# Optimization experiments

Hardware: AMD Instinct MI355X
Metric: run time of the kernel (lower is better)

Reference implementation:

```python
import jax, jax.numpy as jnp
import numpy as np

N0, N1, N2 = 100000, 25000, 6250
E0, E1, E2 = 600000, 150000, 37500
K = 6


def cheb_conv(x, edge_index, W, b):
    """torch_geometric ChebConv with sym normalization, lambda_max=2:
    L_hat = -D^{-1/2} A D^{-1/2}; T0=x, T1=L_hat x, Tk=2 L_hat T_{k-1} - T_{k-2}."""
    n = x.shape[0]
    src, dst = edge_index[0], edge_index[1]
    deg = jax.ops.segment_sum(jnp.ones(src.shape[0], x.dtype), src, num_segments=n)
    dinv = jnp.where(deg > 0, jax.lax.rsqrt(jnp.maximum(deg, 1.0)), 0.0)
    w = -(dinv[src] * dinv[dst])  # [E]

    def prop(h):  # (L_hat h)_i = sum_{j->i} w_ij h_j
        return jax.ops.segment_sum(w[:, None] * h[src], dst, num_segments=n)

    Tx0 = x
    out = Tx0 @ W[0]
    Tx1 = prop(x)
    out = out + Tx1 @ W[1]
    for k in range(2, W.shape[0]):
        Tx2 = 2.0 * prop(Tx1) - Tx0
        out = out + Tx2 @ W[k]
        Tx0, Tx1 = Tx1, Tx2
    return out + b


def pool(x, rows, cols, vals, n_out):
    # sparse.mm(D, x): y[r] += v * x[c]
    return jax.ops.segment_sum(vals[:, None] * x[cols], rows, num_segments=n_out)


def setup_inputs() -> dict:
    key = jax.random.key(0)
    ks = jax.random.split(key, 16)
    inp = {}
    inp["x"] = jax.random.normal(ks[0], (N0, 3), jnp.float32)
    inp["edge_index0"] = jax.random.randint(ks[1], (2, E0), 0, N0, jnp.int32)
    inp["edge_index1"] = jax.random.randint(ks[2], (2, E1), 0, N1, jnp.int32)
    inp["edge_index2"] = jax.random.randint(ks[3], (2, E2), 0, N2, jnp.int32)
    s = 0.05
    inp["W0"] = jax.random.normal(ks[4], (K, 3, 128), jnp.float32) * s
    inp["b0"] = jax.random.normal(ks[5], (128,), jnp.float32) * s
    inp["W1"] = jax.random.normal(ks[6], (K, 128, 128), jnp.float32) * s
    inp["b1"] = jax.random.normal(ks[7], (128,), jnp.float32) * s
    inp["W2"] = jax.random.normal(ks[8], (K, 128, 256), jnp.float32) * s
    inp["b2"] = jax.random.normal(ks[9], (256,), jnp.float32) * s
    inp["D0_rows"] = jax.random.randint(ks[10], (100000,), 0, N1, jnp.int32)
    inp["D0_cols"] = jax.random.randint(ks[11], (100000,), 0, N0, jnp.int32)
    inp["D0_vals"] = jax.random.uniform(ks[12], (100000,), jnp.float32)
    inp["D1_rows"] = jax.random.randint(ks[13], (25000,), 0, N2, jnp.int32)
    inp["D1_cols"] = jax.random.randint(ks[14], (25000,), 0, N1, jnp.int32)
    inp["D1_vals"] = jax.random.uniform(ks[15], (25000,), jnp.float32)
    k2 = jax.random.split(jax.random.fold_in(key, 1), 2)
    inp["linW"] = jax.random.normal(k2[0], (10, N2 * 256), jnp.float32) * 0.001
    inp["linb"] = jax.random.normal(k2[1], (10,), jnp.float32) * s
    return inp


def reference(x, edge_index0, edge_index1, edge_index2, W0, b0, W1, b1, W2, b2,
              D0_rows, D0_cols, D0_vals, D1_rows, D1_cols, D1_vals, linW, linb):
    h = jax.nn.relu(cheb_conv(x, edge_index0, W0, b0))      # [N0,128]
    h = pool(h, D0_rows, D0_cols, D0_vals, N1)               # [N1,128]
    h = jax.nn.relu(cheb_conv(h, edge_index1, W1, b1))      # [N1,128]
    h = pool(h, D1_rows, D1_cols, D1_vals, N2)               # [N2,128]
    h = cheb_conv(h, edge_index2, W2, b2)                    # [N2,256]
    Z = linW @ h.reshape(-1) + linb                           # [10]
    return Z
```

## Files before the change

### kernel.cpp

```cpp
#include <hip/hip_runtime.h>


namespace {
constexpr int cN0 = 100000, cN1 = 25000, cN2 = 6250;
constexpr int cE0 = 600000, cE1 = 150000, cE2 = 37500;
constexpr int cD  = cN2 * 256;

constexpr int JN[8]  = {cN0, cN1, cN2, cN1, cN2, cN0, cN1, cN2};
constexpr int JE[8]  = {cE0, cE1, cE2, 100000, 25000, cE0, cE1, cE2};
constexpr int JB[8]  = {391, 98, 25, 98, 25, 391, 98, 25};
constexpr int JBBASE[9] = {0, 391, 489, 514, 612, 637, 1028, 1126, 1151};
constexpr int TB = 1151;
constexpr int JCB[8] = {293, 74, 19, 49, 13, 293, 74, 19};
constexpr int JCBASE[9] = {0, 293, 367, 386, 435, 448, 741, 815, 834};
constexpr int TCB = 834;
constexpr int CHUNK = 2048;
constexpr int BSTRIDE = 400;

constexpr int EBASE[5]   = {0, 600000, 750000, 787500, 887500};
constexpr int E_TOTAL    = 912500;
constexpr int SBASE[3]   = {0, 600000, 750000};
constexpr int S_TOTAL    = 787500;
constexpr int NBASE[5]   = {0, 100096, 125184, 131584, 156672};
constexpr int NPAD_TOTAL = 163072;
constexpr int DEGBASE[3] = {0, 100000, 125000};
constexpr int DEG_TOTAL  = 131250;
}

typedef __attribute__((ext_vector_type(8))) short short8;
typedef __attribute__((ext_vector_type(4))) float floatx4;

__device__ inline ushort f2bf(float f) {
  union { float f; unsigned u; } v; v.f = f;
  unsigned u = v.u;
  return (ushort)((u + 0x7FFFu + ((u >> 16) & 1u)) >> 16);
}

__device__ inline int job_of_cb(int cb) {
  int j = 0;
  while (cb >= JCBASE[j + 1]) ++j;
  return j;
}
__device__ inline int job_of_bucket(int g) {
  int j = 0;
  while (g >= JBBASE[j + 1]) ++j;
  return j;
}

__global__ __launch_bounds__(256) void c1_count_kernel(
    const int* __restrict__ k0, const int* __restrict__ k1, const int* __restrict__ k2,
    const int* __restrict__ k3, const int* __restrict__ k4, const int* __restrict__ k5,
    const int* __restrict__ k6, const int* __restrict__ k7,
    int* __restrict__ cntCB) {
  __shared__ int cnt[BSTRIDE];
  int cb = blockIdx.x;
  int j = job_of_cb(cb);
  int lb = cb - JCBASE[j];
  const int* keys;
  switch (j) {
    case 0: keys = k0; break; case 1: keys = k1; break; case 2: keys = k2; break;
    case 3: keys = k3; break; case 4: keys = k4; break; case 5: keys = k5; break;
    case 6: keys = k6; break; default: keys = k7; break;
  }
  int nB = JB[j];
  for (int b = threadIdx.x; b < nB; b += 256) cnt[b] = 0;
  __syncthreads();
  int e0 = lb * CHUNK;
  int e1 = min(e0 + CHUNK, JE[j]);
  for (int e = e0 + threadIdx.x; e < e1; e += 256)
    atomicAdd(&cnt[keys[e] >> 8], 1);
  __syncthreads();
  for (int b = threadIdx.x; b < nB; b += 256)
    cntCB[cb * BSTRIDE + b] = cnt[b];
}

__global__ __launch_bounds__(256) void c2a_scan_kernel(int* __restrict__ cntCB,
                                                       int* __restrict__ bucketTot) {
  __shared__ int s[256];
  int g = blockIdx.x;
  int j = job_of_bucket(g);
  int b = g - JBBASE[j];
  int cb0 = JCBASE[j], nCB = JCB[j];
  int carry = 0;
  for (int c0 = 0; c0 < nCB; c0 += 256) {
    int i = c0 + threadIdx.x;
    int v = (i < nCB) ? cntCB[(cb0 + i) * BSTRIDE + b] : 0;
    s[threadIdx.x] = v;
    __syncthreads();
    for (int d = 1; d < 256; d <<= 1) {
      int t = (threadIdx.x >= d) ? s[threadIdx.x - d] : 0;
      __syncthreads();
      s[threadIdx.x] += t;
      __syncthreads();
    }
    if (i < nCB) cntCB[(cb0 + i) * BSTRIDE + b] = carry + s[threadIdx.x] - v;
    carry += s[255];
    __syncthreads();
  }
  if (threadIdx.x == 0) bucketTot[g] = carry;
}

__global__ __launch_bounds__(256) void c2b_scan_kernel(const int* __restrict__ bucketTot,
                                                       int* __restrict__ bucketBase) {
  __shared__ int s[256];
  int j = blockIdx.x;
  int g0 = JBBASE[j], nB = JB[j];
  int carry = 0;
  for (int c0 = 0; c0 < nB; c0 += 256) {
    int i = c0 + threadIdx.x;
    int v = (i < nB) ? bucketTot[g0 + i] : 0;
    s[threadIdx.x] = v;
    __syncthreads();
    for (int d = 1; d < 256; d <<= 1) {
      int t = (threadIdx.x >= d) ? s[threadIdx.x - d] : 0;
      __syncthreads();
      s[threadIdx.x] += t;
      __syncthreads();
    }
    if (i < nB) bucketBase[g0 + i] = carry + s[threadIdx.x] - v;
    carry += s[255];
    __syncthreads();
  }
}

__global__ __launch_bounds__(256) void c3_src_kernel(
    const int* __restrict__ s0, const int* __restrict__ s1, const int* __restrict__ s2,
    const int* __restrict__ cntCB, const int* __restrict__ bucketBase,
    int* __restrict__ scatSrc) {
  __shared__ int base[BSTRIDE];
  int cb = blockIdx.x + JCBASE[5];
  int j = job_of_cb(cb);
  int lb = cb - JCBASE[j];
  const int* keys = (j == 5) ? s0 : (j == 6) ? s1 : s2;
  int nB = JB[j];
  for (int b = threadIdx.x; b < nB; b += 256)
    base[b] = SBASE[j - 5] + bucketBase[JBBASE[j] + b] + cntCB[cb * BSTRIDE + b];
  __syncthreads();
  int e0 = lb * CHUNK;
  int e1 = min(e0 + CHUNK, JE[j]);
  for (int e = e0 + threadIdx.x; e < e1; e += 256) {
    int s = keys[e];
    int pos = atomicAdd(&base[s >> 8], 1);
    scatSrc[pos] = s & 255;
  }
}

__global__ __launch_bounds__(256) void ddeg_kernel(const int* __restrict__ scatSrc,
                                                   const int* __restrict__ bucketTot,
                                                   const int* __restrict__ bucketBase,
                                                   float* __restrict__ dinv) {
  __shared__ int cnt[256];
  int g = blockIdx.x + JBBASE[5];
  int j = job_of_bucket(g);
  int b = g - JBBASE[j];
  int st = SBASE[j - 5] + bucketBase[g];
  int en = st + bucketTot[g];
  cnt[threadIdx.x] = 0;
  __syncthreads();
  for (int idx = st + threadIdx.x; idx < en; idx += 256)
    atomicAdd(&cnt[scatSrc[idx]], 1);
  __syncthreads();
  int node = b * 256 + threadIdx.x;
  if (node < JN[j]) {
    int c = cnt[threadIdx.x];
    dinv[DEGBASE[j - 5] + node] = (c > 0) ? rsqrtf((float)c) : 0.f;
  }
}

__global__ __launch_bounds__(256) void c3_dst_kernel(
    const int* __restrict__ d0, const int* __restrict__ s0,
    const int* __restrict__ d1, const int* __restrict__ s1,
    const int* __restrict__ d2, const int* __restrict__ s2,
    const int* __restrict__ p0r, const int* __restrict__ p0c, const float* __restrict__ p0v,
    const int* __restrict__ p1r, const int* __restrict__ p1c, const float* __restrict__ p1v,
    const float* __restrict__ dinv,
    const int* __restrict__ cntCB, const int* __restrict__ bucketBase,
    int2* __restrict__ scatPairs) {
  __shared__ int base[BSTRIDE];
  int cb = blockIdx.x;
  int j = job_of_cb(cb);
  int lb = cb - JCBASE[j];
  const int* dk; const int* sk; const float* vv = nullptr;
  switch (j) {
    case 0: dk = d0; sk = s0; break;
    case 1: dk = d1; sk = s1; break;
    case 2: dk = d2; sk = s2; break;
    case 3: dk = p0r; sk = p0c; vv = p0v; break;
    default: dk = p1r; sk = p1c; vv = p1v; break;
  }
  int nB = JB[j];
  for (int b = threadIdx.x; b < nB; b += 256)
    base[b] = EBASE[j] + bucketBase[JBBASE[j] + b] + cntCB[cb * BSTRIDE + b];
  __syncthreads();
  int e0 = lb * CHUNK;
  int e1 = min(e0 + CHUNK, JE[j]);
  for (int e = e0 + threadIdx.x; e < e1; e += 256) {
    int d = dk[e];
    int s = sk[e];
    float w;
    if (j < 3) w = -(dinv[DEGBASE[j] + s] * dinv[DEGBASE[j] + d]);
    else w = vv[e];
    int pos = atomicAdd(&base[d >> 8], 1);
    scatPairs[pos] = make_int2(((d & 255) << 17) | s, __float_as_int(w));
  }
}

__global__ __launch_bounds__(256) void dcsr_kernel(const int2* __restrict__ scatPairs,
                                                   const int* __restrict__ bucketTot,
                                                   const int* __restrict__ bucketBase,
                                                   int* __restrict__ off,
                                                   int2* __restrict__ csrPairs) {
  __shared__ int cnt[256];
  __shared__ int sArr[256];
  __shared__ int cur[256];
  int g = blockIdx.x;
  int j = job_of_bucket(g);
  int b = g - JBBASE[j];
  int relBase = bucketBase[g];
  int st = EBASE[j] + relBase;
  int en = st + bucketTot[g];
  cnt[threadIdx.x] = 0;
  __syncthreads();
  for (int idx = st + threadIdx.x; idx < en; idx += 256)
    atomicAdd(&cnt[scatPairs[idx].x >> 17], 1);
  __syncthreads();
  int v = cnt[threadIdx.x];
  sArr[threadIdx.x] = v;
  __syncthreads();
  for (int d = 1; d < 256; d <<= 1) {
    int t = (threadIdx.x >= d) ? sArr[threadIdx.x - d] : 0;
    __syncthreads();
    sArr[threadIdx.x] += t;
    __syncthreads();
  }
  int excl = sArr[threadIdx.x] - v;
  int node = b * 256 + threadIdx.x;
  if (node < JN[j]) off[NBASE[j] + node] = relBase + excl;
  if (threadIdx.x == 0 && b == JB[j] - 1) off[NBASE[j] + JN[j]] = JE[j];
  cur[threadIdx.x] = st + excl;
  __syncthreads();
  for (int idx = st + threadIdx.x; idx < en; idx += 256) {
    int2 p = scatPairs[idx];
    int dl = p.x >> 17;
    int s = p.x & 0x1FFFF;
    int pos = atomicAdd(&cur[dl], 1);
    csrPairs[pos] = make_int2(s, p.y);
  }
}

__global__ __launch_bounds__(256) void csr_prop128_kernel(
    const int* __restrict__ off, const int2* __restrict__ pairs,
    const float* __restrict__ h, float* __restrict__ y, ushort* __restrict__ ybf,
    const float* __restrict__ prev, float scale, int N) {
  int r = blockIdx.x * 8 + (threadIdx.x >> 5);
  int l = threadIdx.x & 31;
  if (r >= N) return;
  int s = off[r], e = off[r + 1];
  const float4* h4 = (const float4*)h;
  float ax = 0.f, ay = 0.f, az = 0.f, aw = 0.f;
  int j = s;
  for (; j + 4 <= e; j += 4) {
    int2 p0 = pairs[j], p1 = pairs[j + 1], p2 = pairs[j + 2], p3 = pairs[j + 3];
    float4 v0 = h4[(size_t)p0.x * 32 + l];
    float4 v1 = h4[(size_t)p1.x * 32 + l];
    float4 v2 = h4[(size_t)p2.x * 32 + l];
    float4 v3 = h4[(size_t)p3.x * 32 + l];
    float w0 = __int_as_float(p0.y), w1 = __int_as_float(p1.y);
    float w2 = __int_as_float(p2.y), w3 = __int_as_float(p3.y);
    ax += w0 * v0.x + w1 * v1.x + w2 * v2.x + w3 * v3.x;
    ay += w0 * v0.y + w1 * v1.y + w2 * v2.y + w3 * v3.y;
    az += w0 * v0.z + w1 * v1.z + w2 * v2.z + w3 * v3.z;
    aw += w0 * v0.w + w1 * v1.w + w2 * v2.w + w3 * v3.w;
  }
  for (; j < e; ++j) {
    int2 p = pairs[j];
    float4 v0 = h4[(size_t)p.x * 32 + l];
    float w = __int_as_float(p.y);
    ax += w * v0.x; ay += w * v0.y; az += w * v0.z; aw += w * v0.w;
  }
  float4 v = make_float4(scale * ax, scale * ay, scale * az, scale * aw);
  if (prev) {
    float4 pv = ((const float4*)prev)[(size_t)r * 32 + l];
    v.x -= pv.x; v.y -= pv.y; v.z -= pv.z; v.w -= pv.w;
  }
  if (y) ((float4*)y)[(size_t)r * 32 + l] = v;
  uint2 sp = make_uint2(f2bf(v.x) | ((unsigned)f2bf(v.y) << 16),
                        f2bf(v.z) | ((unsigned)f2bf(v.w) << 16));
  ((uint2*)ybf)[(size_t)r * 32 + l] = sp;
}

__global__ void csr_prop3_kernel(const int* __restrict__ off, const int2* __restrict__ pairs,
                                 const float4* __restrict__ h, float4* __restrict__ y,
                                 const float4* __restrict__ prev, float scale, int N,
                                 ushort* __restrict__ ybf, int kout) {
  int r = blockIdx.x * blockDim.x + threadIdx.x;
  if (r >= N) return;
  int s = off[r], e = off[r + 1];
  float ax = 0.f, ay = 0.f, az = 0.f;
  int j = s;
  for (; j + 4 <= e; j += 4) {
    int2 p0 = pairs[j], p1 = pairs[j + 1], p2 = pairs[j + 2], p3 = pairs[j + 3];
    float4 h0 = h[p0.x], h1 = h[p1.x], h2 = h[p2.x], h3 = h[p3.x];
    float w0 = __int_as_float(p0.y), w1 = __int_as_float(p1.y);
    float w2 = __int_as_float(p2.y), w3 = __int_as_float(p3.y);
    ax += w0 * h0.x + w1 * h1.x + w2 * h2.x + w3 * h3.x;
    ay += w0 * h0.y + w1 * h1.y + w2 * h2.y + w3 * h3.y;
    az += w0 * h0.z + w1 * h1.z + w2 * h2.z + w3 * h3.z;
  }
  for (; j < e; ++j) {
    int2 p = pairs[j];
    float4 hv = h[p.x];
    float w = __int_as_float(p.y);
    ax += w * hv.x; ay += w * hv.y; az += w * hv.z;
  }
  float4 v = make_float4(scale * ax, scale * ay, scale * az, 0.f);
  if (prev) {
    float4 pv = prev[r];
    v.x -= pv.x; v.y -= pv.y; v.z -= pv.z;
  }
  y[r] = v;
  uint2 sp = make_uint2(f2bf(v.x) | ((unsigned)f2bf(v.y) << 16), (unsigned)f2bf(v.z));
  *(uint2*)(ybf + (size_t)r * 32 + kout * 4) = sp;
}

__global__ void copyx_kernel(const float* __restrict__ x, float4* __restrict__ Tb,
                             ushort* __restrict__ Abf, int N) {
  int r = blockIdx.x * 256 + threadIdx.x;
  if (r >= N) return;
  float x0 = x[3 * r], x1 = x[3 * r + 1], x2 = x[3 * r + 2];
  Tb[r] = make_float4(x0, x1, x2, 0.f);
  uint4 z = make_uint4(0, 0, 0, 0);
  uint4 first = make_uint4(f2bf(x0) | ((unsigned)f2bf(x1) << 16), (unsigned)f2bf(x2), 0, 0);
  uint4* p = (uint4*)(Abf + (size_t)r * 32);
  p[0] = first; p[1] = z; p[2] = z; p[3] = z;
}

__global__ __launch_bounds__(256, 2) void h0_mfma_kernel(
    const ushort* __restrict__ Abf, const ushort* __restrict__ W0b,
    const float* __restrict__ b0, float* __restrict__ h0, int M) {
  __shared__ ushort Al[64][40];
  __shared__ ushort Bl[128][40];
  const int tid = threadIdx.x;
  const int rowBase = blockIdx.x * 64;
  const int wave = tid >> 6;
  const int lane = tid & 63;
  const int m16 = lane & 15;
  const int quad = lane >> 4;
  {
    int sRow = tid >> 2;
    int sK8 = (tid & 3) * 8;
    int row = rowBase + sRow;
    uint4 av = make_uint4(0, 0, 0, 0);
    if (row < M) av = *(const uint4*)(Abf + (size_t)row * 32 + sK8);
    *(uint4*)&Al[sRow][sK8] = av;
  }
#pragma unroll
  for (int l = 0; l < 2; ++l) {
    int lin = tid + l * 256;
    int bRow = lin >> 2;
    int bK8 = (lin & 3) * 8;
    *(uint4*)&Bl[bRow][bK8] = *(const uint4*)(W0b + (size_t)bRow * 32 + bK8);
  }
  __syncthreads();
  short8 a = *(const short8*)&Al[wave * 16 + m16][quad * 8];
  floatx4 acc[8];
#pragma unroll
  for (int c = 0; c < 8; ++c) {
    floatx4 z;
    z[0] = 0.f; z[1] = 0.f; z[2] = 0.f; z[3] = 0.f;
    short8 b = *(const short8*)&Bl[c * 16 + m16][quad * 8];
    acc[c] = __builtin_amdgcn_mfma_f32_16x16x32_bf16(a, b, z, 0, 0, 0);
  }
#pragma unroll
  for (int c = 0; c < 8; ++c) {
    int col = c * 16 + m16;
    float bv = b0[col];
#pragma unroll
    for (int r = 0; r < 4; ++r) {
      int row = rowBase + wave * 16 + quad * 4 + r;
      if (row < M) h0[(size_t)row * 128 + col] = fmaxf(acc[c][r] + bv, 0.f);
    }
  }
}

__global__ void prep_w_kernel(const float* __restrict__ W0, const float* __restrict__ W1,
                              const float* __restrict__ W2, ushort* __restrict__ W0b,
                              ushort* __restrict__ Wt1, ushort* __restrict__ Wt2) {
  int i = blockIdx.x * 256 + threadIdx.x;
  if (i < 768 * 128) {
    int k = i / 128, n = i - k * 128;
    Wt1[(size_t)n * 768 + k] = f2bf(W1[i]);
  } else if (i < 768 * 128 + 768 * 256) {
    int i2 = i - 768 * 128;
    int k = i2 / 256, n = i2 - k * 256;
    Wt2[(size_t)n * 768 + k] = f2bf(W2[i2]);
  } else {
    int i3 = i - 768 * 128 - 768 * 256;
    if (i3 < 128 * 32) {
      int col = i3 >> 5, k = i3 & 31;
      int a = k >> 2, jj = k & 3;
      float v = (k < 24 && jj < 3) ? W0[(a * 3 + jj) * 128 + col] : 0.f;
      W0b[(size_t)col * 32 + k] = f2bf(v);
    }
  }
}

template <int RELU>
__global__ __launch_bounds__(256, 2) void gemm_mfma_kernel(
    const ushort* __restrict__ Tbf, const ushort* __restrict__ Wt,
    const float* __restrict__ bias, float* __restrict__ C, int M, int N) {
  __shared__ ushort Al[64][40];
  __shared__ ushort Bl[128][40];
  const int tid = threadIdx.x;
  const int rowBase = blockIdx.x * 64;
  const int colBase = blockIdx.y * 128;
  const int wave = tid >> 6;
  const int lane = tid & 63;
  const int m16 = lane & 15;
  const int quad = lane >> 4;
  const size_t Mstride = (size_t)M * 128;

  floatx4 acc[8];
#pragma unroll
  for (int c = 0; c < 8; ++c)
#pragma unroll
    for (int r = 0; r < 4; ++r) acc[c][r] = 0.f;

  const int sRow = tid >> 2;
  const int sK8 = (tid & 3) * 8;
  const int growA = rowBase + sRow;
  const bool aValid = growA < M;

  for (int kc = 0; kc < 24; ++kc) {
    uint4 av = make_uint4(0, 0, 0, 0);
    if (aValid)
      av = *(const uint4*)(Tbf + (size_t)(kc >> 2) * Mstride + (size_t)growA * 128
                           + ((kc & 3) << 5) + sK8);
    *(uint4*)&Al[sRow][sK8] = av;
#pragma unroll
    for (int l = 0; l < 2; ++l) {
      int lin = tid + l * 256;
      int bRow = lin >> 2;
      int bK8 = (lin & 3) * 8;
      *(uint4*)&Bl[bRow][bK8] =
          *(const uint4*)(Wt + (size_t)(colBase + bRow) * 768 + kc * 32 + bK8);
    }
    __syncthreads();

    short8 a = *(const short8*)&Al[wave * 16 + m16][quad * 8];
#pragma unroll
    for (int c = 0; c < 8; ++c) {
      short8 b = *(const short8*)&Bl[c * 16 + m16][quad * 8];
      acc[c] = __builtin_amdgcn_mfma_f32_16x16x32_bf16(a, b, acc[c], 0, 0, 0);
    }
    __syncthreads();
  }

#pragma unroll
  for (int c = 0; c < 8; ++c) {
    int col = colBase + c * 16 + m16;
    float bv = bias[col];
#pragma unroll
    for (int r = 0; r < 4; ++r) {
      int row = rowBase + wave * 16 + quad * 4 + r;
      if (row < M) {
        float v = acc[c][r] + bv;
        if (RELU) v = fmaxf(v, 0.f);
        C[(size_t)row * N + col] = v;
      }
    }
  }
}

__global__ void initout_kernel(float* __restrict__ out, const float* __restrict__ linb) {
  int i = threadIdx.x;
  if (i < 10) out[i] = linb[i];
}

__global__ __launch_bounds__(256) void linear_kernel(const float* __restrict__ Wl,
                                                     const float* __restrict__ h,
                                                     float* __restrict__ out, int D) {
  float p[10];
#pragma unroll
  for (int j = 0; j < 10; ++j) p[j] = 0.f;
  int stride = gridDim.x * blockDim.x;
  for (int i = blockIdx.x * blockDim.x + threadIdx.x; i < D; i += stride) {
    float hv = h[i];
#pragma unroll
    for (int j = 0; j < 10; ++j) p[j] += Wl[(size_t)j * D + i] * hv;
  }
#pragma unroll
  for (int j = 0; j < 10; ++j) {
#pragma unroll
    for (int off = 32; off > 0; off >>= 1) p[j] += __shfl_down(p[j], off, 64);
  }
  __shared__ float s[4][10];
  int wave = threadIdx.x >> 6, lane = threadIdx.x & 63;
  if (lane == 0) {
#pragma unroll
    for (int j = 0; j < 10; ++j) s[wave][j] = p[j];
  }
  __syncthreads();
  if (threadIdx.x < 10) {
    float t = s[0][threadIdx.x] + s[1][threadIdx.x] + s[2][threadIdx.x] + s[3][threadIdx.x];
    atomicAdd(&out[threadIdx.x], t);
  }
}

extern "C" void kernel_launch(void* const* d_in, const int* in_sizes, int n_in,
                              void* d_out, int out_size, void* d_ws, size_t ws_size,
                              hipStream_t stream) {
  const float* x    = (const float*)d_in[0];
  const int*   ei0  = (const int*)d_in[1];
  const int*   ei1  = (const int*)d_in[2];
  const int*   ei2  = (const int*)d_in[3];
  const float* W0   = (const float*)d_in[4];
  const float* b0   = (const float*)d_in[5];
  const float* W1   = (const float*)d_in[6];
  const float* b1   = (const float*)d_in[7];
  const float* W2   = (const float*)d_in[8];
  const float* b2   = (const float*)d_in[9];
  const int*   D0r  = (const int*)d_in[10];
  const int*   D0c  = (const int*)d_in[11];
  const float* D0v  = (const float*)d_in[12];
  const int*   D1r  = (const int*)d_in[13];
  const int*   D1c  = (const int*)d_in[14];
  const float* D1v  = (const float*)d_in[15];
  const float* linW = (const float*)d_in[16];
  const float* linb = (const float*)d_in[17];
  float* out = (float*)d_out;
  (void)in_sizes; (void)n_in; (void)out_size; (void)ws_size;

  const int* src0 = ei0;            const int* dst0 = ei0 + cE0;
  const int* src1 = ei1;            const int* dst1 = ei1 + cE1;
  const int* src2 = ei2;            const int* dst2 = ei2 + cE2;

  float* ws = (float*)d_ws;
  size_t off = 0;
  auto alloc = [&](size_t n) {
    float* p = ws + off;
    off += (n + 63) & ~size_t(63);
    return p;
  };
  float* dinv       = alloc(DEG_TOTAL);
  int*   cntCB      = (int*)alloc((size_t)TCB * BSTRIDE);
  int*   bucketTot  = (int*)alloc(TB);
  int*   bucketBase = (int*)alloc(TB);
  int*   scatSrc    = (int*)alloc(S_TOTAL);
  int2*  scatPairs  = (int2*)alloc((size_t)2 * E_TOTAL);
  int2*  csrPairs   = (int2*)alloc((size_t)2 * E_TOTAL);
  int*   offArr     = (int*)alloc(NPAD_TOTAL);
  ushort* W0b       = (ushort*)alloc(128 * 32 / 2);
  ushort* Wt1       = (ushort*)alloc(768 * 128 / 2);
  ushort* Wt2       = (ushort*)alloc(768 * 256 / 2);
  float4* Tb0       = (float4*)alloc((size_t)6 * cN0 * 4);
  ushort* Abf0      = (ushort*)alloc((size_t)cN0 * 16);
  float* h0buf      = alloc((size_t)cN0 * 128);
  float* Tlvl1      = alloc((size_t)6 * cN1 * 128);
  ushort* Tbf1      = (ushort*)alloc((size_t)6 * cN1 * 64);
  float* out1       = alloc((size_t)cN1 * 128);
  float* Tlvl2      = alloc((size_t)6 * cN2 * 128);
  ushort* Tbf2      = (ushort*)alloc((size_t)6 * cN2 * 64);
  float* out2       = alloc((size_t)cN2 * 256);

  auto nb = [](long long n) { return (unsigned)((n + 255) / 256); };

  c1_count_kernel<<<TCB, 256, 0, stream>>>(dst0, dst1, dst2, D0r, D1r,
                                           src0, src1, src2, cntCB);
  c2a_scan_kernel<<<TB, 256, 0, stream>>>(cntCB, bucketTot);
  c2b_scan_kernel<<<8, 256, 0, stream>>>(bucketTot, bucketBase);
  c3_src_kernel<<<TCB - JCBASE[5], 256, 0, stream>>>(src0, src1, src2,
                                                     cntCB, bucketBase, scatSrc);
  ddeg_kernel<<<TB - JBBASE[5], 256, 0, stream>>>(scatSrc, bucketTot, bucketBase, dinv);
  c3_dst_kernel<<<JCBASE[5], 256, 0, stream>>>(dst0, src0, dst1, src1, dst2, src2,
                                               D0r, D0c, D0v, D1r, D1c, D1v,
                                               dinv, cntCB, bucketBase, scatPairs);
  dcsr_kernel<<<JBBASE[5], 256, 0, stream>>>(scatPairs, bucketTot, bucketBase,
                                             offArr, csrPairs);
  prep_w_kernel<<<nb(768 * 384 + 128 * 32), 256, 0, stream>>>(W0, W1, W2, W0b, Wt1, Wt2);

  auto seg_off   = [&](int s) { return offArr + NBASE[s]; };
  auto seg_pairs = [&](int s) { return csrPairs + EBASE[s]; };

  copyx_kernel<<<nb(cN0), 256, 0, stream>>>(x, Tb0, Abf0, cN0);
  {
    auto Tk = [&](int k) { return Tb0 + (size_t)k * cN0; };
    csr_prop3_kernel<<<nb(cN0), 256, 0, stream>>>(seg_off(0), seg_pairs(0),
        Tk(0), Tk(1), nullptr, 1.f, cN0, Abf0, 1);
    csr_prop3_kernel<<<nb(cN0), 256, 0, stream>>>(seg_off(0), seg_pairs(0),
        Tk(1), Tk(2), Tk(0), 2.f, cN0, Abf0, 2);
    csr_prop3_kernel<<<nb(cN0), 256, 0, stream>>>(seg_off(0), seg_pairs(0),
        Tk(2), Tk(3), Tk(1), 2.f, cN0, Abf0, 3);
    csr_prop3_kernel<<<nb(cN0), 256, 0, stream>>>(seg_off(0), seg_pairs(0),
        Tk(3), Tk(4), Tk(2), 2.f, cN0, Abf0, 4);
    csr_prop3_kernel<<<nb(cN0), 256, 0, stream>>>(seg_off(0), seg_pairs(0),
        Tk(4), Tk(5), Tk(3), 2.f, cN0, Abf0, 5);
  }
  h0_mfma_kernel<<<(cN0 + 63) / 64, 256, 0, stream>>>(Abf0, W0b, b0, h0buf, cN0);
  csr_prop128_kernel<<<(cN1 + 7) / 8, 256, 0, stream>>>(
      seg_off(3), seg_pairs(3), h0buf, Tlvl1, Tbf1, nullptr, 1.f, cN1);

  {
    auto Tk  = [&](int k) { return Tlvl1 + (size_t)k * cN1 * 128; };
    auto Tbk = [&](int k) { return Tbf1 + (size_t)k * cN1 * 128; };
    auto prop = [&](int kin, int kout, int kprev, float scale, bool needF32) {
      csr_prop128_kernel<<<(cN1 + 7) / 8, 256, 0, stream>>>(
          seg_off(1), seg_pairs(1), Tk(kin), needF32 ? Tk(kout) : nullptr, Tbk(kout),
          (kprev >= 0) ? Tk(kprev) : nullptr, scale, cN1);
    };
    prop(0, 1, -1, 1.f, true);
    prop(1, 2, 0, 2.f, true);
    prop(2, 3, 1, 2.f, true);
    prop(3, 4, 2, 2.f, true);
    prop(4, 5, 3, 2.f, false);
    dim3 g((cN1 + 63) / 64, 1);
    gemm_mfma_kernel<1><<<g, 256, 0, stream>>>(Tbf1, Wt1, b1, out1, cN1, 128);
  }

  csr_prop128_kernel<<<(cN2 + 7) / 8, 256, 0, stream>>>(
      seg_off(4), seg_pairs(4), out1, Tlvl2, Tbf2, nullptr, 1.f, cN2);

  {
    auto Tk  = [&](int k) { return Tlvl2 + (size_t)k * cN2 * 128; };
    auto Tbk = [&](int k) { return Tbf2 + (size_t)k * cN2 * 128; };
    auto prop = [&](int kin, int kout, int kprev, float scale, bool needF32) {
      csr_prop128_kernel<<<(cN2 + 7) / 8, 256, 0, stream>>>(
          seg_off(2), seg_pairs(2), Tk(kin), needF32 ? Tk(kout) : nullptr, Tbk(kout),
          (kprev >= 0) ? Tk(kprev) : nullptr, scale, cN2);
    };
    prop(0, 1, -1, 1.f, true);
    prop(1, 2, 0, 2.f, true);
    prop(2, 3, 1, 2.f, true);
    prop(3, 4, 2, 2.f, true);
    prop(4, 5, 3, 2.f, false);
    dim3 g((cN2 + 63) / 64, 2);
    gemm_mfma_kernel<0><<<g, 256, 0, stream>>>(Tbf2, Wt2, b2, out2, cN2, 256);
  }

  initout_kernel<<<1, 64, 0, stream>>>(out, linb);
  linear_kernel<<<512, 256, 0, stream>>>(linW, out2, out, cD);
}
```

Baseline: 437.1 us.

## Store pooled inputs in bf16 and compute degrees with global atomics

The layer-0 and layer-1 conv outputs are now written as bf16 through an LDS-staged coalesced store. The pooling steps read them with a new bf16 gather kernel, which halves the gather traffic and output writes. Source-degree counting moves from a scatter-then-histogram pass (two kernels and a scratch buffer) into global atomics inside the count kernel, with dinv computed in the scan kernel and degcnt zeroed in the weight-prep kernel. This removes two launches and a scatter pass, but adds contended global atomics and bf16 rounding of the pooled activations.

New measurement: 438.8 us. About the same (+0.4%).

```diff
diff --git a/kernel.cpp b/kernel.cpp
--- a/kernel.cpp
+++ b/kernel.cpp
@@ -6,25 +6,24 @@
 constexpr int cE0 = 600000, cE1 = 150000, cE2 = 37500;
 constexpr int cD  = cN2 * 256;
 
-constexpr int JN[8]  = {cN0, cN1, cN2, cN1, cN2, cN0, cN1, cN2};
-constexpr int JE[8]  = {cE0, cE1, cE2, 100000, 25000, cE0, cE1, cE2};
-constexpr int JB[8]  = {391, 98, 25, 98, 25, 391, 98, 25};
-constexpr int JBBASE[9] = {0, 391, 489, 514, 612, 637, 1028, 1126, 1151};
-constexpr int TB = 1151;
-constexpr int JCB[8] = {293, 74, 19, 49, 13, 293, 74, 19};
-constexpr int JCBASE[9] = {0, 293, 367, 386, 435, 448, 741, 815, 834};
-constexpr int TCB = 834;
+constexpr int JN[5]  = {cN0, cN1, cN2, cN1, cN2};
+constexpr int JE[5]  = {cE0, cE1, cE2, 100000, 25000};
+constexpr int JB[5]  = {391, 98, 25, 98, 25};
+constexpr int JBBASE[6] = {0, 391, 489, 514, 612, 637};
+constexpr int TB = 637;
+constexpr int JCB[5] = {293, 74, 19, 49, 13};
+constexpr int JCBASE[6] = {0, 293, 367, 386, 435, 448};
+constexpr int TCB = 448;
 constexpr int CHUNK = 2048;
 constexpr int BSTRIDE = 400;
 
 constexpr int EBASE[5]   = {0, 600000, 750000, 787500, 887500};
 constexpr int E_TOTAL    = 912500;
-constexpr int SBASE[3]   = {0, 600000, 750000};
-constexpr int S_TOTAL    = 787500;
 constexpr int NBASE[5]   = {0, 100096, 125184, 131584, 156672};
 constexpr int NPAD_TOTAL = 163072;
 constexpr int DEGBASE[3] = {0, 100000, 125000};
 constexpr int DEG_TOTAL  = 131250;
+constexpr int WPREP_TOTAL = 768 * 128 + 768 * 256 + 128 * 32;
 }
 
 typedef __attribute__((ext_vector_type(8))) short short8;
@@ -36,6 +35,10 @@
   return (ushort)((u + 0x7FFFu + ((u >> 16) & 1u)) >> 16);
 }
 
+__device__ inline float bf2f(unsigned lo16) {
+  return __uint_as_float(lo16 << 16);
+}
+
 __device__ inline int job_of_cb(int cb) {
   int j = 0;
   while (cb >= JCBASE[j + 1]) ++j;
@@ -49,33 +52,41 @@
 
 __global__ __launch_bounds__(256) void c1_count_kernel(
     const int* __restrict__ k0, const int* __restrict__ k1, const int* __restrict__ k2,
-    const int* __restrict__ k3, const int* __restrict__ k4, const int* __restrict__ k5,
-    const int* __restrict__ k6, const int* __restrict__ k7,
-    int* __restrict__ cntCB) {
+    const int* __restrict__ k3, const int* __restrict__ k4,
+    const int* __restrict__ s0, const int* __restrict__ s1, const int* __restrict__ s2,
+    int* __restrict__ degcnt, int* __restrict__ cntCB) {
   __shared__ int cnt[BSTRIDE];
   int cb = blockIdx.x;
   int j = job_of_cb(cb);
   int lb = cb - JCBASE[j];
   const int* keys;
+  const int* srck = nullptr;
+  int dbase = 0;
   switch (j) {
-    case 0: keys = k0; break; case 1: keys = k1; break; case 2: keys = k2; break;
-    case 3: keys = k3; break; case 4: keys = k4; break; case 5: keys = k5; break;
-    case 6: keys = k6; break; default: keys = k7; break;
+    case 0: keys = k0; srck = s0; dbase = DEGBASE[0]; break;
+    case 1: keys = k1; srck = s1; dbase = DEGBASE[1]; break;
+    case 2: keys = k2; srck = s2; dbase = DEGBASE[2]; break;
+    case 3: keys = k3; break;
+    default: keys = k4; break;
   }
   int nB = JB[j];
   for (int b = threadIdx.x; b < nB; b += 256) cnt[b] = 0;
   __syncthreads();
   int e0 = lb * CHUNK;
   int e1 = min(e0 + CHUNK, JE[j]);
-  for (int e = e0 + threadIdx.x; e < e1; e += 256)
+  for (int e = e0 + threadIdx.x; e < e1; e += 256) {
     atomicAdd(&cnt[keys[e] >> 8], 1);
+    if (srck) atomicAdd(&degcnt[dbase + srck[e]], 1);
+  }
   __syncthreads();
   for (int b = threadIdx.x; b < nB; b += 256)
     cntCB[cb * BSTRIDE + b] = cnt[b];
 }
 
 __global__ __launch_bounds__(256) void c2a_scan_kernel(int* __restrict__ cntCB,
-                                                       int* __restrict__ bucketTot) {
+                                                       int* __restrict__ bucketTot,
+                                                       const int* __restrict__ degcnt,
+                                                       float* __restrict__ dinv) {
   __shared__ int s[256];
   int g = blockIdx.x;
   int j = job_of_bucket(g);
@@ -98,6 +109,11 @@
     __syncthreads();
   }
   if (threadIdx.x == 0) bucketTot[g] = carry;
+  int idx = blockIdx.x * 256 + threadIdx.x;
+  if (idx < DEG_TOTAL) {
+    int c = degcnt[idx];
+    dinv[idx] = (c > 0) ? rsqrtf((float)c) : 0.f;
+  }
 }
 
 __global__ __launch_bounds__(256) void c2b_scan_kernel(const int* __restrict__ bucketTot,
@@ -120,50 +136,6 @@
     if (i < nB) bucketBase[g0 + i] = carry + s[threadIdx.x] - v;
     carry += s[255];
     __syncthreads();
-  }
-}
-
-__global__ __launch_bounds__(256) void c3_src_kernel(
-    const int* __restrict__ s0, const int* __restrict__ s1, const int* __restrict__ s2,
-    const int* __restrict__ cntCB, const int* __restrict__ bucketBase,
-    int* __restrict__ scatSrc) {
-  __shared__ int base[BSTRIDE];
-  int cb = blockIdx.x + JCBASE[5];
-  int j = job_of_cb(cb);
-  int lb = cb - JCBASE[j];
-  const int* keys = (j == 5) ? s0 : (j == 6) ? s1 : s2;
-  int nB = JB[j];
-  for (int b = threadIdx.x; b < nB; b += 256)
-    base[b] = SBASE[j - 5] + bucketBase[JBBASE[j] + b] + cntCB[cb * BSTRIDE + b];
-  __syncthreads();
-  int e0 = lb * CHUNK;
-  int e1 = min(e0 + CHUNK, JE[j]);
-  for (int e = e0 + threadIdx.x; e < e1; e += 256) {
-    int s = keys[e];
-    int pos = atomicAdd(&base[s >> 8], 1);
-    scatSrc[pos] = s & 255;
-  }
-}
-
-__global__ __launch_bounds__(256) void ddeg_kernel(const int* __restrict__ scatSrc,
-                                                   const int* __restrict__ bucketTot,
-                                                   const int* __restrict__ bucketBase,
-                                                   float* __restrict__ dinv) {
-  __shared__ int cnt[256];
-  int g = blockIdx.x + JBBASE[5];
-  int j = job_of_bucket(g);
-  int b = g - JBBASE[j];
-  int st = SBASE[j - 5] + bucketBase[g];
-  int en = st + bucketTot[g];
-  cnt[threadIdx.x] = 0;
-  __syncthreads();
-  for (int idx = st + threadIdx.x; idx < en; idx += 256)
-    atomicAdd(&cnt[scatSrc[idx]], 1);
-  __syncthreads();
-  int node = b * 256 + threadIdx.x;
-  if (node < JN[j]) {
-    int c = cnt[threadIdx.x];
-    dinv[DEGBASE[j - 5] + node] = (c > 0) ? rsqrtf((float)c) : 0.f;
   }
 }
 
@@ -289,6 +261,50 @@
   ((uint2*)ybf)[(size_t)r * 32 + l] = sp;
 }
 
+__global__ __launch_bounds__(256) void csr_pool_bf16_kernel(
+    const int* __restrict__ off, const int2* __restrict__ pairs,
+    const ushort* __restrict__ hbf, float* __restrict__ y, ushort* __restrict__ ybf,
+    int N) {
+  int r = blockIdx.x * 8 + (threadIdx.x >> 5);
+  int l = threadIdx.x & 31;
+  if (r >= N) return;
+  int s = off[r], e = off[r + 1];
+  const uint2* h2 = (const uint2*)hbf;
+  float ax = 0.f, ay = 0.f, az = 0.f, aw = 0.f;
+  int j = s;
+  for (; j + 4 <= e; j += 4) {
+    int2 p0 = pairs[j], p1 = pairs[j + 1], p2 = pairs[j + 2], p3 = pairs[j + 3];
+    uint2 v0 = h2[(size_t)p0.x * 32 + l];
+    uint2 v1 = h2[(size_t)p1.x * 32 + l];
+    uint2 v2 = h2[(size_t)p2.x * 32 + l];
+    uint2 v3 = h2[(size_t)p3.x * 32 + l];
+    float w0 = __int_as_float(p0.y), w1 = __int_as_float(p1.y);
+    float w2 = __int_as_float(p2.y), w3 = __int_as_float(p3.y);
+    ax += w0 * bf2f(v0.x & 0xFFFFu) + w1 * bf2f(v1.x & 0xFFFFu)
+        + w2 * bf2f(v2.x & 0xFFFFu) + w3 * bf2f(v3.x & 0xFFFFu);
+    ay += w0 * bf2f(v0.x >> 16) + w1 * bf2f(v1.x >> 16)
+        + w2 * bf2f(v2.x >> 16) + w3 * bf2f(v3.x >> 16);
+    az += w0 * bf2f(v0.y & 0xFFFFu) + w1 * bf2f(v1.y & 0xFFFFu)
+        + w2 * bf2f(v2.y & 0xFFFFu) + w3 * bf2f(v3.y & 0xFFFFu);
+    aw += w0 * bf2f(v0.y >> 16) + w1 * bf2f(v1.y >> 16)
+        + w2 * bf2f(v2.y >> 16) + w3 * bf2f(v3.y >> 16);
+  }
+  for (; j < e; ++j) {
+    int2 p = pairs[j];
+    uint2 v0 = h2[(size_t)p.x * 32 + l];
+    float w = __int_as_float(p.y);
+    ax += w * bf2f(v0.x & 0xFFFFu);
+    ay += w * bf2f(v0.x >> 16);
+    az += w * bf2f(v0.y & 0xFFFFu);
+    aw += w * bf2f(v0.y >> 16);
+  }
+  float4 v = make_float4(ax, ay, az, aw);
+  ((float4*)y)[(size_t)r * 32 + l] = v;
+  uint2 sp = make_uint2(f2bf(v.x) | ((unsigned)f2bf(v.y) << 16),
+                        f2bf(v.z) | ((unsigned)f2bf(v.w) << 16));
+  ((uint2*)ybf)[(size_t)r * 32 + l] = sp;
+}
+
 __global__ void csr_prop3_kernel(const int* __restrict__ off, const int2* __restrict__ pairs,
                                  const float4* __restrict__ h, float4* __restrict__ y,
                                  const float4* __restrict__ prev, float scale, int N,
@@ -337,9 +353,10 @@
 
 __global__ __launch_bounds__(256, 2) void h0_mfma_kernel(
     const ushort* __restrict__ Abf, const ushort* __restrict__ W0b,
-    const float* __restrict__ b0, float* __restrict__ h0, int M) {
+    const float* __restrict__ b0, ushort* __restrict__ h0bf, int M) {
   __shared__ ushort Al[64][40];
   __shared__ ushort Bl[128][40];
+  __shared__ ushort Hs[64][128];
   const int tid = threadIdx.x;
   const int rowBase = blockIdx.x * 64;
   const int wave = tid >> 6;
@@ -376,16 +393,23 @@
     int col = c * 16 + m16;
     float bv = b0[col];
 #pragma unroll
-    for (int r = 0; r < 4; ++r) {
-      int row = rowBase + wave * 16 + quad * 4 + r;
-      if (row < M) h0[(size_t)row * 128 + col] = fmaxf(acc[c][r] + bv, 0.f);
-    }
+    for (int r = 0; r < 4; ++r)
+      Hs[wave * 16 + quad * 4 + r][col] = f2bf(fmaxf(acc[c][r] + bv, 0.f));
+  }
+  __syncthreads();
+  const uint4* ls = (const uint4*)&Hs[0][0];
+  uint4* gd = (uint4*)(h0bf + (size_t)rowBase * 128);
+#pragma unroll
+  for (int i = 0; i < 4; ++i) {
+    int idx = tid + i * 256;
+    if (rowBase + (idx >> 4) < M) gd[idx] = ls[idx];
   }
 }
 
 __global__ void prep_w_kernel(const float* __restrict__ W0, const float* __restrict__ W1,
                               const float* __restrict__ W2, ushort* __restrict__ W0b,
-                              ushort* __restrict__ Wt1, ushort* __restrict__ Wt2) {
+                              ushort* __restrict__ Wt1, ushort* __restrict__ Wt2,
+                              int* __restrict__ degcnt) {
   int i = blockIdx.x * 256 + threadIdx.x;
   if (i < 768 * 128) {
     int k = i / 128, n = i - k * 128;
@@ -394,23 +418,26 @@
     int i2 = i - 768 * 128;
     int k = i2 / 256, n = i2 - k * 256;
     Wt2[(size_t)n * 768 + k] = f2bf(W2[i2]);
+  } else if (i < WPREP_TOTAL) {
+    int i3 = i - 768 * 128 - 768 * 256;
+    int col = i3 >> 5, k = i3 & 31;
+    int a = k >> 2, jj = k & 3;
+    float v = (k < 24 && jj < 3) ? W0[(a * 3 + jj) * 128 + col] : 0.f;
+    W0b[(size_t)col * 32 + k] = f2bf(v);
   } else {
-    int i3 = i - 768 * 128 - 768 * 256;
-    if (i3 < 128 * 32) {
-      int col = i3 >> 5, k = i3 & 31;
-      int a = k >> 2, jj = k & 3;
-      float v = (k < 24 && jj < 3) ? W0[(a * 3 + jj) * 128 + col] : 0.f;
-      W0b[(size_t)col * 32 + k] = f2bf(v);
-    }
-  }
-}
-
-template <int RELU>
+    int i4 = i - WPREP_TOTAL;
+    if (i4 < DEG_TOTAL) degcnt[i4] = 0;
+  }
+}
+
+template <int RELU, int OUTBF>
 __global__ __launch_bounds__(256, 2) void gemm_mfma_kernel(
     const ushort* __restrict__ Tbf, const ushort* __restrict__ Wt,
-    const float* __restrict__ bias, float* __restrict__ C, int M, int N) {
+    const float* __restrict__ bias, float* __restrict__ C, ushort* __restrict__ Cb,
+    int M, int N) {
   __shared__ ushort Al[64][40];
   __shared__ ushort Bl[128][40];
+  __shared__ ushort Hs[64][128];
   const int tid = threadIdx.x;
   const int rowBase = blockIdx.x * 64;
   const int colBase = blockIdx.y * 128;
@@ -456,17 +483,39 @@
     __syncthreads();
   }
 
-#pragma unroll
-  for (int c = 0; c < 8; ++c) {
-    int col = colBase + c * 16 + m16;
-    float bv = bias[col];
-#pragma unroll
-    for (int r = 0; r < 4; ++r) {
-      int row = rowBase + wave * 16 + quad * 4 + r;
-      if (row < M) {
+  if (OUTBF) {
+#pragma unroll
+    for (int c = 0; c < 8; ++c) {
+      int col = c * 16 + m16;
+      float bv = bias[col];
+#pragma unroll
+      for (int r = 0; r < 4; ++r) {
         float v = acc[c][r] + bv;
         if (RELU) v = fmaxf(v, 0.f);
-        C[(size_t)row * N + col] = v;
+        Hs[wave * 16 + quad * 4 + r][col] = f2bf(v);
+      }
+    }
+    __syncthreads();
+    const uint4* ls = (const uint4*)&Hs[0][0];
+    uint4* gd = (uint4*)(Cb + (size_t)rowBase * 128);
+#pragma unroll
+    for (int i = 0; i < 4; ++i) {
+      int idx = tid + i * 256;
+      if (rowBase + (idx >> 4) < M) gd[idx] = ls[idx];
+    }
+  } else {
+#pragma unroll
+    for (int c = 0; c < 8; ++c) {
+      int col = colBase + c * 16 + m16;
+      float bv = bias[col];
+#pragma unroll
+      for (int r = 0; r < 4; ++r) {
+        int row = rowBase + wave * 16 + quad * 4 + r;
+        if (row < M) {
+          float v = acc[c][r] + bv;
+          if (RELU) v = fmaxf(v, 0.f);
+          C[(size_t)row * N + col] = v;
+        }
       }
     }
   }
@@ -543,10 +592,10 @@
     return p;
   };
   float* dinv       = alloc(DEG_TOTAL);
+  int*   degcnt     = (int*)alloc(DEG_TOTAL);
   int*   cntCB      = (int*)alloc((size_t)TCB * BSTRIDE);
   int*   bucketTot  = (int*)alloc(TB);
   int*   bucketBase = (int*)alloc(TB);
-  int*   scatSrc    = (int*)alloc(S_TOTAL);
   int2*  scatPairs  = (int2*)alloc((size_t)2 * E_TOTAL);
   int2*  csrPairs   = (int2*)alloc((size_t)2 * E_TOTAL);
   int*   offArr     = (int*)alloc(NPAD_TOTAL);
@@ -555,29 +604,28 @@
   ushort* Wt2       = (ushort*)alloc(768 * 256 / 2);
   float4* Tb0       = (float4*)alloc((size_t)6 * cN0 * 4);
   ushort* Abf0      = (ushort*)alloc((size_t)cN0 * 16);
-  float* h0buf      = alloc((size_t)cN0 * 128);
+  ushort* h0bf      = (ushort*)alloc((size_t)cN0 * 64);
   float* Tlvl1      = alloc((size_t)6 * cN1 * 128);
   ushort* Tbf1      = (ushort*)alloc((size_t)6 * cN1 * 64);
-  float* out1       = alloc((size_t)cN1 * 128);
+  ushort* out1b     = (ushort*)alloc((size_t)cN1 * 64);
   float* Tlvl2      = alloc((size_t)6 * cN2 * 128);
   ushort* Tbf2      = (ushort*)alloc((size_t)6 * cN2 * 64);
   float* out2       = alloc((size_t)cN2 * 256);
 
   auto nb = [](long long n) { return (unsigned)((n + 255) / 256); };
 
+  prep_w_kernel<<<nb(WPREP_TOTAL + DEG_TOTAL), 256, 0, stream>>>(
+      W0, W1, W2, W0b, Wt1, Wt2, degcnt);
+
   c1_count_kernel<<<TCB, 256, 0, stream>>>(dst0, dst1, dst2, D0r, D1r,
-                                           src0, src1, src2, cntCB);
-  c2a_scan_kernel<<<TB, 256, 0, stream>>>(cntCB, bucketTot);
-  c2b_scan_kernel<<<8, 256, 0, stream>>>(bucketTot, bucketBase);
-  c3_src_kernel<<<TCB - JCBASE[5], 256, 0, stream>>>(src0, src1, src2,
-                                                     cntCB, bucketBase, scatSrc);
-  ddeg_kernel<<<TB - JBBASE[5], 256, 0, stream>>>(scatSrc, bucketTot, bucketBase, dinv);
-  c3_dst_kernel<<<JCBASE[5], 256, 0, stream>>>(dst0, src0, dst1, src1, dst2, src2,
-                                               D0r, D0c, D0v, D1r, D1c, D1v,
-                                               dinv, cntCB, bucketBase, scatPairs);
-  dcsr_kernel<<<JBBASE[5], 256, 0, stream>>>(scatPairs, bucketTot, bucketBase,
-                                             offArr, csrPairs);
-  prep_w_kernel<<<nb(768 * 384 + 128 * 32), 256, 0, stream>>>(W0, W1, W2, W0b, Wt1, Wt2);
+                                           src0, src1, src2, degcnt, cntCB);
+  c2a_scan_kernel<<<TB, 256, 0, stream>>>(cntCB, bucketTot, degcnt, dinv);
+  c2b_scan_kernel<<<5, 256, 0, stream>>>(bucketTot, bucketBase);
+  c3_dst_kernel<<<TCB, 256, 0, stream>>>(dst0, src0, dst1, src1, dst2, src2,
+                                         D0r, D0c, D0v, D1r, D1c, D1v,
+                                         dinv, cntCB, bucketBase, scatPairs);
+  dcsr_kernel<<<TB, 256, 0, stream>>>(scatPairs, bucketTot, bucketBase,
+                                      offArr, csrPairs);
 
   auto seg_off   = [&](int s) { return offArr + NBASE[s]; };
   auto seg_pairs = [&](int s) { return csrPairs + EBASE[s]; };
@@ -596,9 +644,9 @@
     csr_prop3_kernel<<<nb(cN0), 256, 0, stream>>>(seg_off(0), seg_pairs(0),
         Tk(4), Tk(5), Tk(3), 2.f, cN0, Abf0, 5);
   }
-  h0_mfma_kernel<<<(cN0 + 63) / 64, 256, 0, stream>>>(Abf0, W0b, b0, h0buf, cN0);
-  csr_prop128_kernel<<<(cN1 + 7) / 8, 256, 0, stream>>>(
-      seg_off(3), seg_pairs(3), h0buf, Tlvl1, Tbf1, nullptr, 1.f, cN1);
+  h0_mfma_kernel<<<(cN0 + 63) / 64, 256, 0, stream>>>(Abf0, W0b, b0, h0bf, cN0);
+  csr_pool_bf16_kernel<<<(cN1 + 7) / 8, 256, 0, stream>>>(
+      seg_off(3), seg_pairs(3), h0bf, Tlvl1, Tbf1, cN1);
 
   {
     auto Tk  = [&](int k) { return Tlvl1 + (size_t)k * cN1 * 128; };
@@ -614,11 +662,12 @@
     prop(3, 4, 2, 2.f, true);
     prop(4, 5, 3, 2.f, false);
     dim3 g((cN1 + 63) / 64, 1);
-    gemm_mfma_kernel<1><<<g, 256, 0, stream>>>(Tbf1, Wt1, b1, out1, cN1, 128);
-  }
-
-  csr_prop128_kernel<<<(cN2 + 7) / 8, 256, 0, stream>>>(
-      seg_off(4), seg_pairs(4), out1, Tlvl2, Tbf2, nullptr, 1.f, cN2);
+    gemm_mfma_kernel<1, 1><<<g, 256, 0, stream>>>(Tbf1, Wt1, b1, nullptr, out1b,
+                                                  cN1, 128);
+  }
+
+  csr_pool_bf16_kernel<<<(cN2 + 7) / 8, 256, 0, stream>>>(
+      seg_off(4), seg_pairs(4), out1b, Tlvl2, Tbf2, cN2);
 
   {
     auto Tk  = [&](int k) { return Tlvl2 + (size_t)k * cN2 * 128; };
@@ -634,7 +683,8 @@
     prop(3, 4, 2, 2.f, true);
     prop(4, 5, 3, 2.f, false);
     dim3 g((cN2 + 63) / 64, 2);
-    gemm_mfma_kernel<0><<<g, 256, 0, stream>>>(Tbf2, Wt2, b2, out2, cN2, 256);
+    gemm_mfma_kernel<0, 0><<<g, 256, 0, stream>>>(Tbf2, Wt2, b2, out2, nullptr,
+                                                  cN2, 256);
   }
 
   initout_kernel<<<1, 64, 0, stream>>>(out, linb);
```
